# Optimization experiments

Hardware: AMD Instinct MI355X
Metric: run time of the kernel (lower is better)

## Reference

```python
import jax, jax.numpy as jnp
import numpy as np

N = 50000
E = 800000
IN_C = 128
HID = 8
HEADS = 8
OUT_C = 16
NEG_SLOPE = 0.2


def setup_inputs() -> dict:
    key = jax.random.key(0)
    ks = jax.random.split(key, 10)
    x = jax.random.normal(ks[0], (N, IN_C), dtype=jnp.float32)
    edge_index = jax.random.randint(ks[1], (2, E), 0, N, dtype=jnp.int64)
    # layer 1: GATConv(IN_C, HID, heads=HEADS, concat=True)
    s1 = 1.0 / np.sqrt(IN_C)
    W1 = jax.random.normal(ks[2], (HEADS * HID, IN_C), dtype=jnp.float32) * s1
    att_src1 = jax.random.normal(ks[3], (HEADS, HID), dtype=jnp.float32) * 0.1
    att_dst1 = jax.random.normal(ks[4], (HEADS, HID), dtype=jnp.float32) * 0.1
    b1 = jnp.zeros((HEADS * HID,), dtype=jnp.float32)
    # layer 2: GATConv(HEADS*HID, OUT_C, heads=1, concat=False)
    s2 = 1.0 / np.sqrt(HEADS * HID)
    W2 = jax.random.normal(ks[5], (OUT_C, HEADS * HID), dtype=jnp.float32) * s2
    att_src2 = jax.random.normal(ks[6], (1, OUT_C), dtype=jnp.float32) * 0.1
    att_dst2 = jax.random.normal(ks[7], (1, OUT_C), dtype=jnp.float32) * 0.1
    b2 = jnp.zeros((OUT_C,), dtype=jnp.float32)
    return {"x": x, "edge_index": edge_index, "W1": W1, "att_src1": att_src1,
            "att_dst1": att_dst1, "b1": b1, "W2": W2, "att_src2": att_src2,
            "att_dst2": att_dst2, "b2": b2}


def _gat_conv(x, W, att_src, att_dst, bias, src, dst, concat):
    # x: [N, F_in]; W: [H*C, F_in]; att_*: [H, C]
    H, C = att_src.shape
    h = (x @ W.T).reshape(N, H, C)                       # [N, H, C]
    a_src = jnp.einsum('nhc,hc->nh', h, att_src)          # [N, H]
    a_dst = jnp.einsum('nhc,hc->nh', h, att_dst)          # [N, H]
    e = a_src[src] + a_dst[dst]                           # [Etot, H]
    e = jnp.where(e > 0, e, NEG_SLOPE * e)                # LeakyReLU(0.2)
    # segment softmax over edges grouped by destination node
    m = jax.ops.segment_max(e, dst, num_segments=N)       # [N, H]
    e = jnp.exp(e - m[dst])
    denom = jax.ops.segment_sum(e, dst, num_segments=N)   # [N, H]
    alpha = e / (denom[dst] + 1e-16)                      # [Etot, H]
    msg = alpha[:, :, None] * h[src]                      # [Etot, H, C]
    out = jax.ops.segment_sum(msg, dst, num_segments=N)   # [N, H, C]
    if concat:
        out = out.reshape(N, H * C)
    else:
        out = out.mean(axis=1)
    return out + bias


def reference(x, edge_index, W1, att_src1, att_dst1, b1, W2, att_src2, att_dst2, b2):
    # add self-loops (PyG GATConv default)
    loops = jnp.arange(N, dtype=edge_index.dtype)
    src = jnp.concatenate([edge_index[0], loops])
    dst = jnp.concatenate([edge_index[1], loops])
    h = _gat_conv(x, W1, att_src1, att_dst1, b1, src, dst, concat=True)
    h = jax.nn.elu(h)  # dropout is identity in eval mode
    return _gat_conv(h, W2, att_src2, att_dst2, b2, src, dst, concat=False)
```

## Files before the change

kernel.cpp:

```cpp
#include <hip/hip_runtime.h>
#include <hip/hip_fp16.h>
#include <math.h>

#define NN 50000
#define NE 800000
#define ETOT (NE + NN)
#define INC 128
#define F1 64
#define NH 8
#define OC 16
#define NEG 0.2f
#define BSH 7
#define NBUK 391
#define CHUNK_A 4096
#define NBLK_A ((ETOT + CHUNK_A - 1) / CHUNK_A)
#define NBLK_G1 ((NN + 63) / 64)

__device__ __forceinline__ float leaky(float x){ return x > 0.f ? x : NEG * x; }

__device__ __forceinline__ void getsd(const int* __restrict__ ei, int e, int& s, int& d){
    if (e < NE){ s = ei[e]; d = ei[NE + e]; }
    else { s = e - NE; d = s; }
}


__global__ __launch_bounds__(256) void zero_gbcnt(int* __restrict__ gbcnt){
    int i = blockIdx.x*256 + threadIdx.x;
    if (i < NBUK) gbcnt[i] = 0;
}

__global__ __launch_bounds__(256) void bucket_hist(const int* __restrict__ ei, int* __restrict__ gbcnt){
    __shared__ int bcnt[NBUK];
    int tid = threadIdx.x;
    for (int j = tid; j < NBUK; j += 256) bcnt[j] = 0;
    __syncthreads();
    int e0 = blockIdx.x * CHUNK_A;
    int e1 = e0 + CHUNK_A; if (e1 > ETOT) e1 = ETOT;
    for (int e = e0 + tid; e < e1; e += 256){
        int d = (e < NE) ? ei[NE + e] : e - NE;
        atomicAdd(&bcnt[d >> BSH], 1);
    }
    __syncthreads();
    for (int j = tid; j < NBUK; j += 256)
        if (bcnt[j]) atomicAdd(&gbcnt[j], bcnt[j]);
}

__global__ __launch_bounds__(512) void bucket_scan(const int* __restrict__ gbcnt,
        int* __restrict__ gboff, int* __restrict__ gbcur){
    __shared__ int s[512];
    int t = threadIdx.x;
    int v = (t < NBUK) ? gbcnt[t] : 0;
    s[t] = v; __syncthreads();
    for (int off = 1; off < 512; off <<= 1){
        int u = (t >= off) ? s[t - off] : 0;
        __syncthreads();
        s[t] += u;
        __syncthreads();
    }
    if (t < NBUK){ int ex = s[t] - v; gboff[t] = ex; gbcur[t] = ex; }
    if (t == 0) gboff[NBUK] = ETOT;
}

__global__ __launch_bounds__(256, 4) void scatter_gemm1(const int* __restrict__ ei,
        int* __restrict__ gbcur, unsigned* __restrict__ packed,
        const float* __restrict__ x, const float* __restrict__ W1,
        const float* __restrict__ att_s, const float* __restrict__ att_d,
        __half* __restrict__ h1h, float* __restrict__ a_src, float* __restrict__ a_dst){
    __shared__ int bcnt[NBUK];
    __shared__ float xs[64*144];
    int tid = threadIdx.x;
    if (blockIdx.x < NBLK_A){
        for (int j = tid; j < NBUK; j += 256) bcnt[j] = 0;
        __syncthreads();
        int e0 = blockIdx.x * CHUNK_A;
        int e1 = e0 + CHUNK_A; if (e1 > ETOT) e1 = ETOT;
        for (int e = e0 + tid; e < e1; e += 256){
            int d = (e < NE) ? ei[NE + e] : e - NE;
            atomicAdd(&bcnt[d >> BSH], 1);
        }
        __syncthreads();
        for (int j = tid; j < NBUK; j += 256){
            int c = bcnt[j];
            bcnt[j] = c ? atomicAdd(&gbcur[j], c) : 0;
        }
        __syncthreads();
        for (int e = e0 + tid; e < e1; e += 256){
            int s, d; getsd(ei, e, s, d);
            int pos = atomicAdd(&bcnt[d >> BSH], 1);
            packed[pos] = ((unsigned)s << 16) | (unsigned)d;
        }
        return;
    }
    int base = (blockIdx.x - NBLK_A) * 64;
    int w = tid >> 6, lane = tid & 63;
    int oL = lane >> 2, ks = lane & 3;
    int o1 = (w & 1)*32 + oL, o2 = o1 + 16;
    float4 wra[8], wrb[8];
    {
        const float4* W4 = reinterpret_cast<const float4*>(W1);
        #pragma unroll
        for (int j4 = 0; j4 < 8; ++j4){
            wra[j4] = W4[o1*32 + ks*8 + j4];
            wrb[j4] = W4[o2*32 + ks*8 + j4];
        }
    }
    float as_o1 = att_s[o1], as_o2 = att_s[o2];
    float ad_o1 = att_d[o1], ad_o2 = att_d[o2];
    {
        #pragma unroll
        for (int j = 0; j < 8; ++j){
            int f = tid + 256*j;
            int row = f >> 5, c4 = f & 31;
            int n = base + row;
            float4 v = make_float4(0.f,0.f,0.f,0.f);
            if (n < NN) v = reinterpret_cast<const float4*>(x)[n*32 + c4];
            int sk = c4 >> 3, j4 = c4 & 7;
            *(float4*)(&xs[row*144 + sk*36 + j4*4]) = v;
        }
    }
    __syncthreads();
    int rbase = (w >> 1) * 32;
    int hA = (w & 1)*4 + (oL >> 3);
    for (int r = 0; r < 32; ++r){
        int row = rbase + r;
        const float* xb = &xs[row*144 + ks*36];
        float acc1 = 0.f, acc2 = 0.f;
        #pragma unroll
        for (int j4 = 0; j4 < 8; ++j4){
            float4 xv = *(const float4*)(xb + j4*4);
            acc1 = fmaf(xv.x, wra[j4].x, acc1);
            acc2 = fmaf(xv.x, wrb[j4].x, acc2);
            acc1 = fmaf(xv.y, wra[j4].y, acc1);
            acc2 = fmaf(xv.y, wrb[j4].y, acc2);
            acc1 = fmaf(xv.z, wra[j4].z, acc1);
            acc2 = fmaf(xv.z, wrb[j4].z, acc2);
            acc1 = fmaf(xv.w, wra[j4].w, acc1);
            acc2 = fmaf(xv.w, wrb[j4].w, acc2);
        }
        acc1 += __shfl_xor(acc1, 1); acc1 += __shfl_xor(acc1, 2);
        acc2 += __shfl_xor(acc2, 1); acc2 += __shfl_xor(acc2, 2);
        int node = base + row;
        float p1s = acc1 * as_o1, p2s = acc2 * as_o2;
        float p1d = acc1 * ad_o1, p2d = acc2 * ad_o2;
        p1s += __shfl_xor(p1s, 4); p1s += __shfl_xor(p1s, 8); p1s += __shfl_xor(p1s, 16);
        p2s += __shfl_xor(p2s, 4); p2s += __shfl_xor(p2s, 8); p2s += __shfl_xor(p2s, 16);
        p1d += __shfl_xor(p1d, 4); p1d += __shfl_xor(p1d, 8); p1d += __shfl_xor(p1d, 16);
        p2d += __shfl_xor(p2d, 4); p2d += __shfl_xor(p2d, 8); p2d += __shfl_xor(p2d, 16);
        if (node < NN){
            if (ks == 0){
                h1h[node*64 + o1] = __float2half(acc1);
                h1h[node*64 + o2] = __float2half(acc2);
                if ((oL & 7) == 0){
                    a_src[node*8 + hA]     = p1s;
                    a_dst[node*8 + hA]     = p1d;
                    a_src[node*8 + hA + 2] = p2s;
                    a_dst[node*8 + hA + 2] = p2d;
                }
            }
        }
    }
}

__global__ __launch_bounds__(256) void bucket_finalize(const unsigned* __restrict__ packed,
        const int* __restrict__ gboff, int* __restrict__ rowstart, int* __restrict__ esrc){
    __shared__ int ldeg[1 << BSH];
    __shared__ int lcur[1 << BSH];
    __shared__ int wtot[2];
    int b = blockIdx.x, t = threadIdx.x;
    if (t < (1 << BSH)) ldeg[t] = 0;
    __syncthreads();
    int p0 = gboff[b], p1 = gboff[b+1];
    for (int i = p0 + t; i < p1; i += 256)
        atomicAdd(&ldeg[packed[i] & ((1 << BSH) - 1)], 1);
    __syncthreads();
    if (t < (1 << BSH)){
        int v = ldeg[t];
        int lane = t & 63, w = t >> 6;
        int iv = v;
        #pragma unroll
        for (int off = 1; off < 64; off <<= 1){
            int u = __shfl_up(iv, off);
            if (lane >= off) iv += u;
        }
        lcur[t] = iv;
        if (lane == 63) wtot[w] = iv;
    }
    __syncthreads();
    if (t < (1 << BSH)){
        int v = ldeg[t];
        int w = t >> 6;
        int incl = lcur[t] + (w ? wtot[0] : 0);
        int rs = p0 + incl - v;
        int n = (b << BSH) + t;
        if (n < NN) rowstart[n] = rs;
        lcur[t] = rs;
    }
    if (b == 0 && t == 0) rowstart[NN] = ETOT;
    __syncthreads();
    for (int i = p0 + t; i < p1; i += 256){
        unsigned p = packed[i];
        int pos = atomicAdd(&lcur[p & ((1 << BSH) - 1)], 1);
        esrc[pos] = (int)(p >> 16);
    }
}


__global__ __launch_bounds__(256, 4) void gemm2(const float* __restrict__ out1, const float* __restrict__ W2,
        const float* __restrict__ att_s, const float* __restrict__ att_d,
        __half* __restrict__ h2h, float* __restrict__ a_src, float* __restrict__ a_dst){
    __shared__ float xs[64*80];
    int tid = threadIdx.x;
    int base = blockIdx.x * 64;
    int w = tid >> 6, lane = tid & 63;
    int o = lane >> 2, ks = lane & 3;
    float4 wr[4];
    {
        const float4* W4 = reinterpret_cast<const float4*>(W2);
        #pragma unroll
        for (int j4 = 0; j4 < 4; ++j4)
            wr[j4] = W4[o*16 + ks*4 + j4];
    }
    float as_o = att_s[o], ad_o = att_d[o];
    {
        #pragma unroll
        for (int j = 0; j < 4; ++j){
            int f = tid + 256*j;
            int row = f >> 4, c4 = f & 15;
            int n = base + row;
            float4 v = make_float4(0.f,0.f,0.f,0.f);
            if (n < NN) v = reinterpret_cast<const float4*>(out1)[n*16 + c4];
            v.x = v.x > 0.f ? v.x : __expf(v.x) - 1.f;
            v.y = v.y > 0.f ? v.y : __expf(v.y) - 1.f;
            v.z = v.z > 0.f ? v.z : __expf(v.z) - 1.f;
            v.w = v.w > 0.f ? v.w : __expf(v.w) - 1.f;
            int sk = c4 >> 2, j4 = c4 & 3;
            *(float4*)(&xs[row*80 + sk*20 + j4*4]) = v;
        }
    }
    __syncthreads();
    for (int r = 0; r < 16; ++r){
        int row = w*16 + r;
        const float* xb = &xs[row*80 + ks*20];
        float acc = 0.f;
        #pragma unroll
        for (int j4 = 0; j4 < 4; ++j4){
            float4 xv = *(const float4*)(xb + j4*4);
            acc = fmaf(xv.x, wr[j4].x, acc);
            acc = fmaf(xv.y, wr[j4].y, acc);
            acc = fmaf(xv.z, wr[j4].z, acc);
            acc = fmaf(xv.w, wr[j4].w, acc);
        }
        acc += __shfl_xor(acc, 1); acc += __shfl_xor(acc, 2);
        int node = base + row;
        float ps = acc * as_o, pd = acc * ad_o;
        ps += __shfl_xor(ps, 4); ps += __shfl_xor(ps, 8);
        ps += __shfl_xor(ps, 16); ps += __shfl_xor(ps, 32);
        pd += __shfl_xor(pd, 4); pd += __shfl_xor(pd, 8);
        pd += __shfl_xor(pd, 16); pd += __shfl_xor(pd, 32);
        if (node < NN){
            if (ks == 0) h2h[node*16 + o] = __float2half(acc);
            if (lane == 0){ a_src[node] = ps; a_dst[node] = pd; }
        }
    }
}


__global__ __launch_bounds__(256) void layer1_node(const int* __restrict__ rowstart,
        const int* __restrict__ esrc, const float* __restrict__ a_src,
        const float* __restrict__ a_dst, const __half* __restrict__ h1h,
        const float* __restrict__ b1, float* __restrict__ out1){
    int wid = __builtin_amdgcn_readfirstlane((blockIdx.x*256 + threadIdx.x) >> 6);
    int lane = threadIdx.x & 63;
    if (wid >= NN) return;
    int n = wid;
    int h = lane >> 3;
    int r0 = rowstart[n], r1 = rowstart[n+1];
    float ad = a_dst[n*8 + h];
    float den0 = 0.f, acc0 = 0.f, den1 = 0.f, acc1 = 0.f;
    float den2 = 0.f, acc2 = 0.f, den3 = 0.f, acc3 = 0.f;
    float den4 = 0.f, acc4 = 0.f, den5 = 0.f, acc5 = 0.f;
    float den6 = 0.f, acc6 = 0.f, den7 = 0.f, acc7 = 0.f;
    int i = r0;
    for (; i + 7 < r1; i += 8){
        int s0 = esrc[i],   s1 = esrc[i+1], s2 = esrc[i+2], s3 = esrc[i+3];
        int s4 = esrc[i+4], s5 = esrc[i+5], s6 = esrc[i+6], s7 = esrc[i+7];
        float e0 = leaky(a_src[s0*8 + h] + ad);
        float e1 = leaky(a_src[s1*8 + h] + ad);
        float e2 = leaky(a_src[s2*8 + h] + ad);
        float e3 = leaky(a_src[s3*8 + h] + ad);
        float e4 = leaky(a_src[s4*8 + h] + ad);
        float e5 = leaky(a_src[s5*8 + h] + ad);
        float e6 = leaky(a_src[s6*8 + h] + ad);
        float e7 = leaky(a_src[s7*8 + h] + ad);
        float hv0 = __half2float(h1h[s0*64 + lane]);
        float hv1 = __half2float(h1h[s1*64 + lane]);
        float hv2 = __half2float(h1h[s2*64 + lane]);
        float hv3 = __half2float(h1h[s3*64 + lane]);
        float hv4 = __half2float(h1h[s4*64 + lane]);
        float hv5 = __half2float(h1h[s5*64 + lane]);
        float hv6 = __half2float(h1h[s6*64 + lane]);
        float hv7 = __half2float(h1h[s7*64 + lane]);
        float p0 = __expf(e0), p1 = __expf(e1), p2 = __expf(e2), p3 = __expf(e3);
        float p4 = __expf(e4), p5 = __expf(e5), p6 = __expf(e6), p7 = __expf(e7);
        den0 += p0; acc0 = fmaf(p0, hv0, acc0);
        den1 += p1; acc1 = fmaf(p1, hv1, acc1);
        den2 += p2; acc2 = fmaf(p2, hv2, acc2);
        den3 += p3; acc3 = fmaf(p3, hv3, acc3);
        den4 += p4; acc4 = fmaf(p4, hv4, acc4);
        den5 += p5; acc5 = fmaf(p5, hv5, acc5);
        den6 += p6; acc6 = fmaf(p6, hv6, acc6);
        den7 += p7; acc7 = fmaf(p7, hv7, acc7);
    }
    for (; i + 3 < r1; i += 4){
        int s0 = esrc[i], s1 = esrc[i+1], s2 = esrc[i+2], s3 = esrc[i+3];
        float e0 = leaky(a_src[s0*8 + h] + ad);
        float e1 = leaky(a_src[s1*8 + h] + ad);
        float e2 = leaky(a_src[s2*8 + h] + ad);
        float e3 = leaky(a_src[s3*8 + h] + ad);
        float hv0 = __half2float(h1h[s0*64 + lane]);
        float hv1 = __half2float(h1h[s1*64 + lane]);
        float hv2 = __half2float(h1h[s2*64 + lane]);
        float hv3 = __half2float(h1h[s3*64 + lane]);
        float p0 = __expf(e0), p1 = __expf(e1), p2 = __expf(e2), p3 = __expf(e3);
        den0 += p0; acc0 = fmaf(p0, hv0, acc0);
        den1 += p1; acc1 = fmaf(p1, hv1, acc1);
        den2 += p2; acc2 = fmaf(p2, hv2, acc2);
        den3 += p3; acc3 = fmaf(p3, hv3, acc3);
    }
    for (; i < r1; ++i){
        int s = esrc[i];
        float p = __expf(leaky(a_src[s*8 + h] + ad));
        den0 += p; acc0 = fmaf(p, __half2float(h1h[s*64 + lane]), acc0);
    }
    float den = ((den0 + den1) + (den2 + den3)) + ((den4 + den5) + (den6 + den7));
    float acc = ((acc0 + acc1) + (acc2 + acc3)) + ((acc4 + acc5) + (acc6 + acc7));
    out1[n*64 + lane] = acc/(den + 1e-16f) + b1[lane];
}

__global__ __launch_bounds__(256) void layer2_node(const int* __restrict__ rowstart,
        const int* __restrict__ esrc, const float* __restrict__ a_src,
        const float* __restrict__ a_dst, const __half* __restrict__ h2h,
        const float* __restrict__ b2, float* __restrict__ out){
    int wid = __builtin_amdgcn_readfirstlane((blockIdx.x*256 + threadIdx.x) >> 6);
    int lane = threadIdx.x & 63;
    if (wid >= NN) return;
    int n = wid;
    int slot = lane >> 4, c = lane & 15;
    int r0 = rowstart[n], r1 = rowstart[n+1];
    float ad = a_dst[n];
    float den0 = 0.f, acc0 = 0.f, den1 = 0.f, acc1 = 0.f;
    float den2 = 0.f, acc2 = 0.f, den3 = 0.f, acc3 = 0.f;
    int i = r0 + slot;
    for (; i + 12 < r1; i += 16){
        int s0 = esrc[i], s1 = esrc[i+4], s2 = esrc[i+8], s3 = esrc[i+12];
        float p0 = __expf(leaky(a_src[s0] + ad));
        float p1 = __expf(leaky(a_src[s1] + ad));
        float p2 = __expf(leaky(a_src[s2] + ad));
        float p3 = __expf(leaky(a_src[s3] + ad));
        float hv0 = __half2float(h2h[s0*16 + c]);
        float hv1 = __half2float(h2h[s1*16 + c]);
        float hv2 = __half2float(h2h[s2*16 + c]);
        float hv3 = __half2float(h2h[s3*16 + c]);
        den0 += p0; acc0 = fmaf(p0, hv0, acc0);
        den1 += p1; acc1 = fmaf(p1, hv1, acc1);
        den2 += p2; acc2 = fmaf(p2, hv2, acc2);
        den3 += p3; acc3 = fmaf(p3, hv3, acc3);
    }
    for (; i < r1; i += 4){
        int s = esrc[i];
        float p = __expf(leaky(a_src[s] + ad));
        den0 += p; acc0 = fmaf(p, __half2float(h2h[s*16 + c]), acc0);
    }
    float den = (den0 + den1) + (den2 + den3);
    float acc = (acc0 + acc1) + (acc2 + acc3);
    den += __shfl_xor(den, 16); den += __shfl_xor(den, 32);
    acc += __shfl_xor(acc, 16); acc += __shfl_xor(acc, 32);
    if (slot == 0) out[n*16 + c] = acc/(den + 1e-16f) + b2[c];
}

extern "C" void kernel_launch(void* const* d_in, const int* in_sizes, int n_in,
                              void* d_out, int out_size, void* d_ws, size_t ws_size,
                              hipStream_t stream){
    const float* x    = (const float*)d_in[0];
    const int*   ei   = (const int*)d_in[1];
    const float* W1   = (const float*)d_in[2];
    const float* as1w = (const float*)d_in[3];
    const float* ad1w = (const float*)d_in[4];
    const float* b1   = (const float*)d_in[5];
    const float* W2   = (const float*)d_in[6];
    const float* as2w = (const float*)d_in[7];
    const float* ad2w = (const float*)d_in[8];
    const float* b2   = (const float*)d_in[9];
    float* out = (float*)d_out;

    float* ws = (float*)d_ws;
    __half* h1h     = (__half*)ws;
    float* out1     = ws + (size_t)32*NN;
    int*   rowstart = (int*)(ws + (size_t)96*NN);
    int*   gbcnt    = rowstart + NN + 1;
    int*   gboff    = gbcnt + NBUK;
    int*   gbcur    = gboff + NBUK + 1;
    unsigned* packed= (unsigned*)(gbcur + NBUK);
    int*   esrc     = (int*)(packed + ETOT);
    float* a_src1 = out;
    float* a_dst1 = out + (size_t)8*NN;
    __half* h2h   = h1h;
    float* a_src2 = ws + (size_t)8*NN;
    float* a_dst2 = a_src2 + NN;

    hipLaunchKernelGGL(zero_gbcnt,      dim3(2), dim3(256), 0, stream, gbcnt);
    hipLaunchKernelGGL(bucket_hist,     dim3(NBLK_A), dim3(256), 0, stream, ei, gbcnt);
    hipLaunchKernelGGL(bucket_scan,     dim3(1), dim3(512), 0, stream, gbcnt, gboff, gbcur);
    hipLaunchKernelGGL(scatter_gemm1,   dim3(NBLK_A + NBLK_G1), dim3(256), 0, stream,
                       ei, gbcur, packed, x, W1, as1w, ad1w, h1h, a_src1, a_dst1);
    hipLaunchKernelGGL(bucket_finalize, dim3(NBUK), dim3(256), 0, stream, packed, gboff, rowstart, esrc);

    hipLaunchKernelGGL(layer1_node, dim3((NN*64 + 255)/256), dim3(256), 0, stream,
                       rowstart, esrc, a_src1, a_dst1, h1h, b1, out1);
    hipLaunchKernelGGL(gemm2, dim3((NN + 63)/64), dim3(256), 0, stream, out1, W2, as2w, ad2w, h2h, a_src2, a_dst2);
    hipLaunchKernelGGL(layer2_node, dim3((NN*64 + 255)/256), dim3(256), 0, stream,
                       rowstart, esrc, a_src2, a_dst2, h2h, b2, out);
}
```

Measured before the change: 137.7 us.

## Split fused scatter+gemm1 and restructure gemm1 to keep x rows in registers

Separates the edge bucket scatter from the first-layer GEMM into two kernels and launches the GEMM after bucket finalize. The GEMM is rewritten so W1 is staged in shared memory and each thread holds two x rows in registers, covering 128 nodes per block and looping over all 64 outputs. It also accumulates the attention dot products in registers. This removes the x staging per tile and the 24 shuffles per row, but it loses the overlap of scatter and GEMM in one launch and writes h1h one half at a time with strided stores.

```diff
diff --git a/kernel.cpp b/kernel.cpp
--- a/kernel.cpp
+++ b/kernel.cpp
@@ -14,7 +14,8 @@
 #define NBUK 391
 #define CHUNK_A 4096
 #define NBLK_A ((ETOT + CHUNK_A - 1) / CHUNK_A)
-#define NBLK_G1 ((NN + 63) / 64)
+#define G1TILE 128
+#define NBLK_G1 ((NN + G1TILE - 1) / G1TILE)
 
 __device__ __forceinline__ float leaky(float x){ return x > 0.f ? x : NEG * x; }
 
@@ -61,103 +62,28 @@
     if (t == 0) gboff[NBUK] = ETOT;
 }
 
-__global__ __launch_bounds__(256, 4) void scatter_gemm1(const int* __restrict__ ei,
-        int* __restrict__ gbcur, unsigned* __restrict__ packed,
-        const float* __restrict__ x, const float* __restrict__ W1,
-        const float* __restrict__ att_s, const float* __restrict__ att_d,
-        __half* __restrict__ h1h, float* __restrict__ a_src, float* __restrict__ a_dst){
+__global__ __launch_bounds__(256) void bucket_scatter(const int* __restrict__ ei,
+        int* __restrict__ gbcur, unsigned* __restrict__ packed){
     __shared__ int bcnt[NBUK];
-    __shared__ float xs[64*144];
     int tid = threadIdx.x;
-    if (blockIdx.x < NBLK_A){
-        for (int j = tid; j < NBUK; j += 256) bcnt[j] = 0;
-        __syncthreads();
-        int e0 = blockIdx.x * CHUNK_A;
-        int e1 = e0 + CHUNK_A; if (e1 > ETOT) e1 = ETOT;
-        for (int e = e0 + tid; e < e1; e += 256){
-            int d = (e < NE) ? ei[NE + e] : e - NE;
-            atomicAdd(&bcnt[d >> BSH], 1);
-        }
-        __syncthreads();
-        for (int j = tid; j < NBUK; j += 256){
-            int c = bcnt[j];
-            bcnt[j] = c ? atomicAdd(&gbcur[j], c) : 0;
-        }
-        __syncthreads();
-        for (int e = e0 + tid; e < e1; e += 256){
-            int s, d; getsd(ei, e, s, d);
-            int pos = atomicAdd(&bcnt[d >> BSH], 1);
-            packed[pos] = ((unsigned)s << 16) | (unsigned)d;
-        }
-        return;
-    }
-    int base = (blockIdx.x - NBLK_A) * 64;
-    int w = tid >> 6, lane = tid & 63;
-    int oL = lane >> 2, ks = lane & 3;
-    int o1 = (w & 1)*32 + oL, o2 = o1 + 16;
-    float4 wra[8], wrb[8];
-    {
-        const float4* W4 = reinterpret_cast<const float4*>(W1);
-        #pragma unroll
-        for (int j4 = 0; j4 < 8; ++j4){
-            wra[j4] = W4[o1*32 + ks*8 + j4];
-            wrb[j4] = W4[o2*32 + ks*8 + j4];
-        }
-    }
-    float as_o1 = att_s[o1], as_o2 = att_s[o2];
-    float ad_o1 = att_d[o1], ad_o2 = att_d[o2];
-    {
-        #pragma unroll
-        for (int j = 0; j < 8; ++j){
-            int f = tid + 256*j;
-            int row = f >> 5, c4 = f & 31;
-            int n = base + row;
-            float4 v = make_float4(0.f,0.f,0.f,0.f);
-            if (n < NN) v = reinterpret_cast<const float4*>(x)[n*32 + c4];
-            int sk = c4 >> 3, j4 = c4 & 7;
-            *(float4*)(&xs[row*144 + sk*36 + j4*4]) = v;
-        }
-    }
-    __syncthreads();
-    int rbase = (w >> 1) * 32;
-    int hA = (w & 1)*4 + (oL >> 3);
-    for (int r = 0; r < 32; ++r){
-        int row = rbase + r;
-        const float* xb = &xs[row*144 + ks*36];
-        float acc1 = 0.f, acc2 = 0.f;
-        #pragma unroll
-        for (int j4 = 0; j4 < 8; ++j4){
-            float4 xv = *(const float4*)(xb + j4*4);
-            acc1 = fmaf(xv.x, wra[j4].x, acc1);
-            acc2 = fmaf(xv.x, wrb[j4].x, acc2);
-            acc1 = fmaf(xv.y, wra[j4].y, acc1);
-            acc2 = fmaf(xv.y, wrb[j4].y, acc2);
-            acc1 = fmaf(xv.z, wra[j4].z, acc1);
-            acc2 = fmaf(xv.z, wrb[j4].z, acc2);
-            acc1 = fmaf(xv.w, wra[j4].w, acc1);
-            acc2 = fmaf(xv.w, wrb[j4].w, acc2);
-        }
-        acc1 += __shfl_xor(acc1, 1); acc1 += __shfl_xor(acc1, 2);
-        acc2 += __shfl_xor(acc2, 1); acc2 += __shfl_xor(acc2, 2);
-        int node = base + row;
-        float p1s = acc1 * as_o1, p2s = acc2 * as_o2;
-        float p1d = acc1 * ad_o1, p2d = acc2 * ad_o2;
-        p1s += __shfl_xor(p1s, 4); p1s += __shfl_xor(p1s, 8); p1s += __shfl_xor(p1s, 16);
-        p2s += __shfl_xor(p2s, 4); p2s += __shfl_xor(p2s, 8); p2s += __shfl_xor(p2s, 16);
-        p1d += __shfl_xor(p1d, 4); p1d += __shfl_xor(p1d, 8); p1d += __shfl_xor(p1d, 16);
-        p2d += __shfl_xor(p2d, 4); p2d += __shfl_xor(p2d, 8); p2d += __shfl_xor(p2d, 16);
-        if (node < NN){
-            if (ks == 0){
-                h1h[node*64 + o1] = __float2half(acc1);
-                h1h[node*64 + o2] = __float2half(acc2);
-                if ((oL & 7) == 0){
-                    a_src[node*8 + hA]     = p1s;
-                    a_dst[node*8 + hA]     = p1d;
-                    a_src[node*8 + hA + 2] = p2s;
-                    a_dst[node*8 + hA + 2] = p2d;
-                }
-            }
-        }
+    for (int j = tid; j < NBUK; j += 256) bcnt[j] = 0;
+    __syncthreads();
+    int e0 = blockIdx.x * CHUNK_A;
+    int e1 = e0 + CHUNK_A; if (e1 > ETOT) e1 = ETOT;
+    for (int e = e0 + tid; e < e1; e += 256){
+        int d = (e < NE) ? ei[NE + e] : e - NE;
+        atomicAdd(&bcnt[d >> BSH], 1);
+    }
+    __syncthreads();
+    for (int j = tid; j < NBUK; j += 256){
+        int c = bcnt[j];
+        bcnt[j] = c ? atomicAdd(&gbcur[j], c) : 0;
+    }
+    __syncthreads();
+    for (int e = e0 + tid; e < e1; e += 256){
+        int s, d; getsd(ei, e, s, d);
+        int pos = atomicAdd(&bcnt[d >> BSH], 1);
+        packed[pos] = ((unsigned)s << 16) | (unsigned)d;
     }
 }
 
@@ -201,6 +127,67 @@
         unsigned p = packed[i];
         int pos = atomicAdd(&lcur[p & ((1 << BSH) - 1)], 1);
         esrc[pos] = (int)(p >> 16);
+    }
+}
+
+__global__ __launch_bounds__(256) void gemm1(const float* __restrict__ x, const float* __restrict__ W1,
+        const float* __restrict__ att_s, const float* __restrict__ att_d,
+        __half* __restrict__ h1h, float* __restrict__ a_src, float* __restrict__ a_dst){
+    __shared__ float w1s[F1*144];
+    int tid = threadIdx.x;
+    int base = blockIdx.x * G1TILE;
+    for (int i = tid; i < F1*INC; i += 256){
+        int o = i >> 7, k = i & 127;
+        w1s[o*144 + (k >> 5)*36 + (k & 31)] = W1[o*INC + k];
+    }
+    int w = tid >> 6, lane = tid & 63;
+    int nr = lane >> 2, ks = lane & 3;
+    int node0 = base + w*32 + nr*2;
+    int node1 = node0 + 1;
+    bool v0 = node0 < NN, v1 = node1 < NN;
+    float4 xa[8], xb[8];
+    {
+        const float4* x4 = reinterpret_cast<const float4*>(x);
+        #pragma unroll
+        for (int j = 0; j < 8; ++j){
+            xa[j] = v0 ? x4[node0*32 + ks*8 + j] : make_float4(0.f,0.f,0.f,0.f);
+            xb[j] = v1 ? x4[node1*32 + ks*8 + j] : make_float4(0.f,0.f,0.f,0.f);
+        }
+    }
+    __syncthreads();
+    float ps0 = 0.f, pd0 = 0.f, ps1 = 0.f, pd1 = 0.f;
+    for (int o = 0; o < F1; ++o){
+        const float4* wb = reinterpret_cast<const float4*>(&w1s[o*144 + ks*36]);
+        float d0 = 0.f, d1 = 0.f;
+        #pragma unroll
+        for (int j = 0; j < 8; ++j){
+            float4 wv = wb[j];
+            d0 = fmaf(xa[j].x, wv.x, d0);
+            d1 = fmaf(xb[j].x, wv.x, d1);
+            d0 = fmaf(xa[j].y, wv.y, d0);
+            d1 = fmaf(xb[j].y, wv.y, d1);
+            d0 = fmaf(xa[j].z, wv.z, d0);
+            d1 = fmaf(xb[j].z, wv.z, d1);
+            d0 = fmaf(xa[j].w, wv.w, d0);
+            d1 = fmaf(xb[j].w, wv.w, d1);
+        }
+        d0 += __shfl_xor(d0, 1); d0 += __shfl_xor(d0, 2);
+        d1 += __shfl_xor(d1, 1); d1 += __shfl_xor(d1, 2);
+        float as_o = att_s[o], ad_o = att_d[o];
+        ps0 = fmaf(d0, as_o, ps0); pd0 = fmaf(d0, ad_o, pd0);
+        ps1 = fmaf(d1, as_o, ps1); pd1 = fmaf(d1, ad_o, pd1);
+        if (ks == 0){
+            if (v0) h1h[node0*64 + o] = __float2half(d0);
+            if (v1) h1h[node1*64 + o] = __float2half(d1);
+        }
+        if ((o & 7) == 7){
+            if (ks == 0){
+                int h = o >> 3;
+                if (v0){ a_src[node0*8 + h] = ps0; a_dst[node0*8 + h] = pd0; }
+                if (v1){ a_src[node1*8 + h] = ps1; a_dst[node1*8 + h] = pd1; }
+            }
+            ps0 = 0.f; pd0 = 0.f; ps1 = 0.f; pd1 = 0.f;
+        }
     }
 }
 
@@ -411,10 +398,10 @@
     hipLaunchKernelGGL(zero_gbcnt,      dim3(2), dim3(256), 0, stream, gbcnt);
     hipLaunchKernelGGL(bucket_hist,     dim3(NBLK_A), dim3(256), 0, stream, ei, gbcnt);
     hipLaunchKernelGGL(bucket_scan,     dim3(1), dim3(512), 0, stream, gbcnt, gboff, gbcur);
-    hipLaunchKernelGGL(scatter_gemm1,   dim3(NBLK_A + NBLK_G1), dim3(256), 0, stream,
-                       ei, gbcur, packed, x, W1, as1w, ad1w, h1h, a_src1, a_dst1);
+    hipLaunchKernelGGL(bucket_scatter,  dim3(NBLK_A), dim3(256), 0, stream, ei, gbcur, packed);
     hipLaunchKernelGGL(bucket_finalize, dim3(NBUK), dim3(256), 0, stream, packed, gboff, rowstart, esrc);
 
+    hipLaunchKernelGGL(gemm1, dim3(NBLK_G1), dim3(256), 0, stream, x, W1, as1w, ad1w, h1h, a_src1, a_dst1);
     hipLaunchKernelGGL(layer1_node, dim3((NN*64 + 255)/256), dim3(256), 0, stream,
                        rowstart, esrc, a_src1, a_dst1, h1h, b1, out1);
     hipLaunchKernelGGL(gemm2, dim3((NN + 63)/64), dim3(256), 0, stream, out1, W2, as2w, ad2w, h2h, a_src2, a_dst2);
```

Result: slower. 145.6 us (+5.7%).
